# Optimization experiments

Measured on AMD Instinct MI355X. Metric: run time of the kernel, lower is better.

## Reference

```python
import jax, jax.numpy as jnp
import numpy as np

B, T, D = 2, 2048, 1280
H = 20
DH = D // H  # 64
S_PAST = 2048


def setup_inputs() -> dict:
    key = jax.random.key(0)
    ks = jax.random.split(key, 7)
    return {
        "x": jax.random.normal(ks[0], (B, T, D), dtype=jnp.float32),
        "past_K": jax.random.normal(ks[1], (B, H, S_PAST, DH), dtype=jnp.float32),
        "past_V": jax.random.normal(ks[2], (B, H, S_PAST, DH), dtype=jnp.float32),
        "w_q": jax.random.normal(ks[3], (D, D), dtype=jnp.float32),
        "w_k": jax.random.normal(ks[4], (D, D), dtype=jnp.float32),
        "w_v": jax.random.normal(ks[5], (D, D), dtype=jnp.float32),
        "W_o": jax.random.normal(ks[6], (D, D), dtype=jnp.float32),
    }


def reference(x, past_K, past_V, w_q, w_k, w_v, W_o):
    b, t, _ = x.shape
    # projections
    q = x @ w_q  # [B,T,D]
    k = x @ w_k
    v = x @ w_v
    # split heads -> [B,H,T,DH]
    Q = q.reshape(b, t, H, DH).transpose(0, 2, 1, 3)
    K = k.reshape(b, t, H, DH).transpose(0, 2, 1, 3)
    V = v.reshape(b, t, H, DH).transpose(0, 2, 1, 3)
    # concat KV cache along sequence dim
    K = jnp.concatenate([past_K, K], axis=-2)  # [B,H,S_past+T,DH]
    V = jnp.concatenate([past_V, V], axis=-2)
    # attention (no causal mask, matching the original module)
    scores = jnp.einsum("bhtd,bhsd->bhts", Q, K) / jnp.sqrt(jnp.float32(DH))
    attn = jax.nn.softmax(scores, axis=-1)
    values = jnp.einsum("bhts,bhsd->bhtd", attn, V)  # [B,H,T,DH]
    values = values.transpose(0, 2, 1, 3).reshape(b, t, D)
    out = values @ W_o
    return out, K, V
```

## Files before the change

kernel.cpp:

```cpp
#include <hip/hip_runtime.h>

#define NB 2
#define NH 20
#define TT 2048
#define DD 1280
#define DHH 64
#define SP 2048
#define SS 4096
#define MM (NB*TT)

typedef __attribute__((ext_vector_type(8))) short bf16x8;
typedef __attribute__((ext_vector_type(4))) float f32x4;
typedef unsigned short u16;
typedef unsigned int u32;

__device__ __forceinline__ f32x4 mfma16(bf16x8 a, bf16x8 b, f32x4 c) {
  return __builtin_amdgcn_mfma_f32_16x16x32_bf16(a, b, c, 0, 0, 0);
}

__device__ __forceinline__ u16 f2bf(float f) {
  u32 x = __builtin_bit_cast(u32, f);
  x += 0x7fffu + ((x >> 16) & 1u);
  return (u16)(x >> 16);
}
__device__ __forceinline__ float bf2f(u16 u) {
  u32 x = ((u32)u) << 16;
  return __builtin_bit_cast(float, x);
}

__device__ __forceinline__ float fexp2(float x) {
#if __has_builtin(__builtin_amdgcn_exp2f)
  return __builtin_amdgcn_exp2f(x);
#else
  return exp2f(x);
#endif
}

__device__ __forceinline__ u32 cvtpk(float lo, float hi) {
  u32 r;
  asm("v_cvt_pk_bf16_f32 %0, %1, %2" : "=v"(r) : "v"(lo), "v"(hi));
  return r;
}

template<int ROWS>
__device__ __forceinline__ void stage_swz(char* lds, const u16* __restrict__ gsrc,
                                          int ld, int tid) {
  constexpr int ITER = ROWS * 8 / 256;
#pragma unroll
  for (int i = 0; i < ITER; ++i) {
    int id = i * 256 + tid;
    int row = id >> 3, c = id & 7;
    int cs = c ^ (row & 7);
    const u16* src = gsrc + row * ld + cs * 8;
    __builtin_amdgcn_global_load_lds(
        (const __attribute__((address_space(1))) u32*)src,
        (__attribute__((address_space(3))) u32*)(lds + id * 16), 16, 0, 0);
  }
}

__device__ __forceinline__ void gload16(const u16* src, char* ldst) {
  __builtin_amdgcn_global_load_lds(
      (const __attribute__((address_space(1))) u32*)src,
      (__attribute__((address_space(3))) u32*)ldst, 16, 0, 0);
}

__device__ __forceinline__ bf16x8 frag_swz(const char* lds, int row, int cc) {
  return *(const bf16x8*)(lds + row * 128 + ((cc ^ (row & 7)) << 4));
}

__global__ void splitx(const float* __restrict__ x, u16* __restrict__ xh,
                       u16* __restrict__ xl) {
  int i = blockIdx.x * 256 + threadIdx.x;
  float4 v = ((const float4*)x)[i];
  ushort4 hi, lo;
  hi.x = f2bf(v.x); lo.x = f2bf(v.x - bf2f(hi.x));
  hi.y = f2bf(v.y); lo.y = f2bf(v.y - bf2f(hi.y));
  hi.z = f2bf(v.z); lo.z = f2bf(v.z - bf2f(hi.z));
  hi.w = f2bf(v.w); lo.w = f2bf(v.w - bf2f(hi.w));
  ((ushort4*)xh)[i] = hi;
  ((ushort4*)xl)[i] = lo;
}

__global__ void transw(const float* __restrict__ wq, const float* __restrict__ wk,
                       const float* __restrict__ wv, const float* __restrict__ wo,
                       u16* __restrict__ wqkvh, u16* __restrict__ wqkvl,
                       u16* __restrict__ wot) {
  __shared__ float tile[64][65];
  int mat = blockIdx.z;
  const float* src = mat == 0 ? wq : mat == 1 ? wk : mat == 2 ? wv : wo;
  int k0 = blockIdx.x * 64, n0 = blockIdx.y * 64;
  int tid = threadIdx.x;
#pragma unroll
  for (int rep = 0; rep < 16; ++rep) {
    int id = rep * 256 + tid;
    int kl = id >> 6, nl = id & 63;
    tile[nl][kl] = src[(k0 + kl) * DD + n0 + nl];
  }
  __syncthreads();
#pragma unroll
  for (int rep = 0; rep < 16; ++rep) {
    int id = rep * 256 + tid;
    int nl = id >> 6, kl = id & 63;
    float v = tile[nl][kl];
    u16 hi = f2bf(v);
    if (mat < 3) {
      int idx = (mat * DD + n0 + nl) * DD + k0 + kl;
      wqkvh[idx] = hi;
      wqkvl[idx] = f2bf(v - bf2f(hi));
    } else {
      wot[(n0 + nl) * DD + k0 + kl] = hi;
    }
  }
}

__global__ void pastk(const float* __restrict__ pK, float* __restrict__ dK,
                      u16* __restrict__ Kh, u16* __restrict__ Kl) {
  int i = blockIdx.x * 256 + threadIdx.x;
  int e = i * 4;
  int dh = e & 63;
  int s = (e >> 6) & (SP - 1);
  int bh = e >> 17;
  float4 v = *(const float4*)(pK + e);
  int o = (bh * SS + s) * DHH + dh;
  *(float4*)(dK + o) = v;
  ushort4 hi, lo;
  hi.x = f2bf(v.x); lo.x = f2bf(v.x - bf2f(hi.x));
  hi.y = f2bf(v.y); lo.y = f2bf(v.y - bf2f(hi.y));
  hi.z = f2bf(v.z); lo.z = f2bf(v.z - bf2f(hi.z));
  hi.w = f2bf(v.w); lo.w = f2bf(v.w - bf2f(hi.w));
  *(ushort4*)(Kh + o) = hi;
  *(ushort4*)(Kl + o) = lo;
}

__global__ void pastv(const float* __restrict__ pV, float* __restrict__ dV,
                      u16* __restrict__ Vt) {
  __shared__ u16 tile[64][72];
  int bi = blockIdx.x;
  int bh = bi >> 5, st = bi & 31;
  int s0 = st * 64;
  int tid = threadIdx.x;
  const float* src = pV + (bh * SP + s0) * DHH;
  float* dst = dV + (bh * SS + s0) * DHH;
#pragma unroll
  for (int rep = 0; rep < 16; ++rep) {
    int id = rep * 256 + tid;
    int sl = id >> 6, dh = id & 63;
    float v = src[sl * DHH + dh];
    dst[sl * DHH + dh] = v;
    tile[dh][sl] = f2bf(v);
  }
  __syncthreads();
  u16* vdst = Vt + (bh * DHH) * SS + s0;
#pragma unroll
  for (int rep = 0; rep < 4; ++rep) {
    int id = rep * 256 + tid;
    int dh = id >> 4, s4 = (id & 15) * 4;
    ushort4 vv;
    vv.x = tile[dh][s4];     vv.y = tile[dh][s4 + 1];
    vv.z = tile[dh][s4 + 2]; vv.w = tile[dh][s4 + 3];
    *(ushort4*)(vdst + dh * SS + s4) = vv;
  }
}

__launch_bounds__(256, 2)
__global__ void gemm_qkv(const u16* __restrict__ xh, const u16* __restrict__ xl,
                         const u16* __restrict__ wh, const u16* __restrict__ wl,
                         u16* __restrict__ Qh, u16* __restrict__ Ql,
                         u16* __restrict__ Kh, u16* __restrict__ Kl,
                         u16* __restrict__ Vt,
                         float* __restrict__ dK, float* __restrict__ dV) {
  __shared__ __align__(16) char sm[65536];
  char* Ah = sm;          char* Al = sm + 16384;
  char* Bh = sm + 32768;  char* Bl = sm + 49152;
  int tid = threadIdx.x, lane = tid & 63, w = tid >> 6;
  int wm = w >> 1, wn = w & 1;
  int r15 = lane & 15, grp = lane >> 4;
  int mBase = blockIdx.x * 128;
  int by = blockIdx.y;
  int nGlob = by * 128;
  const bool split = (by < 20);
  f32x4 acc[4][4] = {};
  const u16* aH = xh + mBase * DD;
  const u16* aL = xl + mBase * DD;
  const u16* bH = wh + nGlob * DD;
  const u16* bL = wl + nGlob * DD;
  for (int k0 = 0; k0 < DD; k0 += 64) {
    stage_swz<128>(Ah, aH + k0, DD, tid);
    stage_swz<128>(Bh, bH + k0, DD, tid);
    if (split) {
      stage_swz<128>(Al, aL + k0, DD, tid);
      stage_swz<128>(Bl, bL + k0, DD, tid);
    }
    __syncthreads();
#pragma unroll
    for (int kk = 0; kk < 2; ++kk) {
      int cc = kk * 4 + grp;
      bf16x8 fah[4], fal[4], fbh[4], fbl[4];
#pragma unroll
      for (int i = 0; i < 4; ++i) {
        int ra = wm * 64 + i * 16 + r15;
        fah[i] = frag_swz(Ah, ra, cc);
        int rb = wn * 64 + i * 16 + r15;
        fbh[i] = frag_swz(Bh, rb, cc);
        if (split) {
          fal[i] = frag_swz(Al, ra, cc);
          fbl[i] = frag_swz(Bl, rb, cc);
        }
      }
      if (split) {
#pragma unroll
        for (int i = 0; i < 4; ++i)
#pragma unroll
          for (int j = 0; j < 4; ++j) {
            acc[i][j] = mfma16(fah[i], fbh[j], acc[i][j]);
            acc[i][j] = mfma16(fah[i], fbl[j], acc[i][j]);
            acc[i][j] = mfma16(fal[i], fbh[j], acc[i][j]);
          }
      } else {
#pragma unroll
        for (int i = 0; i < 4; ++i)
#pragma unroll
          for (int j = 0; j < 4; ++j)
            acc[i][j] = mfma16(fah[i], fbh[j], acc[i][j]);
      }
    }
    __syncthreads();
  }
  int proj = by / 10;
  int nb = (by % 10) * 128 + wn * 64;
#pragma unroll
  for (int i = 0; i < 4; ++i)
#pragma unroll
    for (int j = 0; j < 4; ++j)
#pragma unroll
      for (int r = 0; r < 4; ++r) {
        int m = mBase + wm * 64 + i * 16 + grp * 4 + r;
        int n = nb + j * 16 + r15;
        float v = acc[i][j][r];
        int b = m >> 11, t = m & 2047;
        int h = n >> 6, dh = n & 63;
        int bhh = b * NH + h;
        if (proj == 0) {
          float q = v * 0.180336880111f;
          u16 hi = f2bf(q);
          int idx = (bhh * TT + t) * DHH + dh;
          Qh[idx] = hi;
          Ql[idx] = f2bf(q - bf2f(hi));
        } else if (proj == 1) {
          int idx = (bhh * SS + SP + t) * DHH + dh;
          dK[idx] = v;
          u16 hi = f2bf(v);
          Kh[idx] = hi;
          Kl[idx] = f2bf(v - bf2f(hi));
        } else {
          int idx = (bhh * SS + SP + t) * DHH + dh;
          dV[idx] = v;
          Vt[(bhh * DHH + dh) * SS + SP + t] = f2bf(v);
        }
      }
}

__launch_bounds__(256, 2)
__global__ void attn(const u16* __restrict__ Qh, const u16* __restrict__ Ql,
                     const u16* __restrict__ Kh, const u16* __restrict__ Kl,
                     const u16* __restrict__ Vt, u16* __restrict__ ao) {
  __shared__ __align__(16) char Ks[8192];
  __shared__ __align__(16) char Kls[8192];
  __shared__ __align__(16) char Vs[8192];
  __shared__ __align__(16) u16 Pw[4][16][72];
  __shared__ __align__(16) float bc[4][16];
  int bi = blockIdx.x;
  int bh = bi >> 4, qt4 = bi & 15;
  int q0 = qt4 * 128;
  int tid = threadIdx.x, lane = tid & 63, w = tid >> 6;
  int r15 = lane & 15, grp = lane >> 4;
  int qbase = q0 + w * 32;
  bf16x8 fqh[2][2], fql[2][2];
#pragma unroll
  for (int qt = 0; qt < 2; ++qt) {
    int qrow = qbase + qt * 16 + r15;
    const u16* qb = Qh + (bh * TT + qrow) * DHH + grp * 8;
    const u16* qbl = Ql + (bh * TT + qrow) * DHH + grp * 8;
    fqh[qt][0] = *(const bf16x8*)qb;   fqh[qt][1] = *(const bf16x8*)(qb + 32);
    fql[qt][0] = *(const bf16x8*)qbl;  fql[qt][1] = *(const bf16x8*)(qbl + 32);
  }
  float mrun[2] = {-1e30f, -1e30f};
  float lrun[2] = {0.f, 0.f};
  f32x4 oacc[2][4] = {};
  int id0 = tid, id1 = 256 + tid;
  int r0 = id0 >> 3, c0 = id0 & 7;
  int r1 = id1 >> 3, c1 = id1 & 7;
  const u16* kh0 = Kh + bh * SS * DHH + r0 * DHH + (c0 ^ (r0 & 7)) * 8;
  const u16* kh1 = Kh + bh * SS * DHH + r1 * DHH + (c1 ^ (r1 & 7)) * 8;
  const u16* kl0 = Kl + bh * SS * DHH + r0 * DHH + (c0 ^ (r0 & 7)) * 8;
  const u16* kl1 = Kl + bh * SS * DHH + r1 * DHH + (c1 ^ (r1 & 7)) * 8;
  const u16* v0 = Vt + bh * DHH * SS + r0 * SS + (c0 ^ (r0 & 7)) * 8;
  const u16* v1 = Vt + bh * DHH * SS + r1 * SS + (c1 ^ (r1 & 7)) * 8;
  char* dK0 = Ks + id0 * 16;  char* dK1 = Ks + id1 * 16;
  char* dL0 = Kls + id0 * 16; char* dL1 = Kls + id1 * 16;
  char* dV0 = Vs + id0 * 16;  char* dV1 = Vs + id1 * 16;

  for (int it = 0; it < SS / 64; ++it) {
    gload16(kh0, dK0); gload16(kh1, dK1);
    gload16(kl0, dL0); gload16(kl1, dL1);
    gload16(v0, dV0);  gload16(v1, dV1);
    kh0 += 64 * DHH; kh1 += 64 * DHH;
    kl0 += 64 * DHH; kl1 += 64 * DHH;
    v0 += 64; v1 += 64;
    __syncthreads();
#pragma unroll
    for (int qt = 0; qt < 2; ++qt) {
      f32x4 st[4];
      __builtin_amdgcn_s_setprio(1);
#pragma unroll
      for (int kt = 0; kt < 4; ++kt) {
        f32x4 a = {0.f, 0.f, 0.f, 0.f};
#pragma unroll
        for (int ks = 0; ks < 2; ++ks) {
          int cc = ks * 4 + grp;
          bf16x8 kfh = frag_swz(Ks, kt * 16 + r15, cc);
          bf16x8 kfl = frag_swz(Kls, kt * 16 + r15, cc);
          a = mfma16(kfh, fqh[qt][ks], a);
          a = mfma16(kfh, fql[qt][ks], a);
          a = mfma16(kfl, fqh[qt][ks], a);
        }
        st[kt] = a;
      }
      __builtin_amdgcn_s_setprio(0);
      float cm = fmaxf(fmaxf(fmaxf(st[0][0], st[0][1]), fmaxf(st[0][2], st[0][3])),
                       fmaxf(fmaxf(st[1][0], st[1][1]), fmaxf(st[1][2], st[1][3])));
      cm = fmaxf(cm, fmaxf(fmaxf(fmaxf(st[2][0], st[2][1]), fmaxf(st[2][2], st[2][3])),
                           fmaxf(fmaxf(st[3][0], st[3][1]), fmaxf(st[3][2], st[3][3]))));
      cm = fmaxf(cm, __shfl_xor(cm, 16));
      cm = fmaxf(cm, __shfl_xor(cm, 32));
      if (!__all(cm <= mrun[qt] + 8.f)) {
        float mnew = fmaxf(mrun[qt], cm);
        float sc = fexp2(mrun[qt] - mnew);
        lrun[qt] *= sc;
        mrun[qt] = mnew;
        if (grp == 0) bc[w][r15] = sc;
        f32x4 scv = *(const f32x4*)&bc[w][grp * 4];
#pragma unroll
        for (int d = 0; d < 4; ++d) {
          oacc[qt][d][0] *= scv[0]; oacc[qt][d][1] *= scv[1];
          oacc[qt][d][2] *= scv[2]; oacc[qt][d][3] *= scv[3];
        }
      }
      float m = mrun[qt];
      float ps = 0.f;
#pragma unroll
      for (int kt = 0; kt < 4; ++kt)
#pragma unroll
        for (int r = 0; r < 4; ++r) {
          float p = fexp2(st[kt][r] - m);
          st[kt][r] = p;
          ps += p;
        }
      ps += __shfl_xor(ps, 16);
      ps += __shfl_xor(ps, 32);
      lrun[qt] += ps;
#pragma unroll
      for (int kt = 0; kt < 4; ++kt) {
        u32 w0 = cvtpk(st[kt][0], st[kt][1]);
        u32 w1 = cvtpk(st[kt][2], st[kt][3]);
        uint2 pk = {w0, w1};
        *(uint2*)&Pw[w][r15][kt * 16 + grp * 4] = pk;
      }
      bf16x8 pa0 = *(const bf16x8*)&Pw[w][r15][grp * 8];
      bf16x8 pa1 = *(const bf16x8*)&Pw[w][r15][32 + grp * 8];
      __builtin_amdgcn_s_setprio(1);
#pragma unroll
      for (int d = 0; d < 4; ++d) {
        bf16x8 vf0 = frag_swz(Vs, d * 16 + r15, grp);
        bf16x8 vf1 = frag_swz(Vs, d * 16 + r15, 4 + grp);
        oacc[qt][d] = mfma16(pa0, vf0, oacc[qt][d]);
        oacc[qt][d] = mfma16(pa1, vf1, oacc[qt][d]);
      }
      __builtin_amdgcn_s_setprio(0);
    }
    __syncthreads();
  }
  int b = bh / NH, h = bh % NH;
#pragma unroll
  for (int qt = 0; qt < 2; ++qt) {
    float inv = 1.0f / lrun[qt];
    if (grp == 0) bc[w][r15] = inv;
    f32x4 li = *(const f32x4*)&bc[w][grp * 4];
#pragma unroll
    for (int d = 0; d < 4; ++d)
#pragma unroll
      for (int r = 0; r < 4; ++r) {
        int q = qbase + qt * 16 + grp * 4 + r;
        int col = h * DHH + d * 16 + r15;
        ao[(b * TT + q) * DD + col] = f2bf(oacc[qt][d][r] * li[r]);
      }
  }
}

__launch_bounds__(256, 2)
__global__ void gemm_out(const u16* __restrict__ ao, const u16* __restrict__ wot,
                         float* __restrict__ out) {
  __shared__ __align__(16) char sm[32768];
  char* As = sm;
  char* Bs = sm + 16384;
  int tid = threadIdx.x, lane = tid & 63, w = tid >> 6;
  int wm = w >> 1, wn = w & 1;
  int r15 = lane & 15, grp = lane >> 4;
  int mBase = blockIdx.x * 128, nBase = blockIdx.y * 128;
  f32x4 acc[4][4] = {};
  for (int k0 = 0; k0 < DD; k0 += 64) {
    stage_swz<128>(As, ao + mBase * DD + k0, DD, tid);
    stage_swz<128>(Bs, wot + nBase * DD + k0, DD, tid);
    __syncthreads();
#pragma unroll
    for (int kk = 0; kk < 2; ++kk) {
      int cc = kk * 4 + grp;
      bf16x8 fa[4], fb[4];
#pragma unroll
      for (int i = 0; i < 4; ++i) {
        fa[i] = frag_swz(As, wm * 64 + i * 16 + r15, cc);
        fb[i] = frag_swz(Bs, wn * 64 + i * 16 + r15, cc);
      }
#pragma unroll
      for (int i = 0; i < 4; ++i)
#pragma unroll
        for (int j = 0; j < 4; ++j)
          acc[i][j] = mfma16(fa[i], fb[j], acc[i][j]);
    }
    __syncthreads();
  }
#pragma unroll
  for (int i = 0; i < 4; ++i)
#pragma unroll
    for (int j = 0; j < 4; ++j)
#pragma unroll
      for (int r = 0; r < 4; ++r) {
        int m = mBase + wm * 64 + i * 16 + grp * 4 + r;
        int n = nBase + wn * 64 + j * 16 + r15;
        out[m * DD + n] = acc[i][j][r];
      }
}

extern "C" void kernel_launch(void* const* d_in, const int* in_sizes, int n_in,
                              void* d_out, int out_size, void* d_ws, size_t ws_size,
                              hipStream_t stream) {
  const float* x  = (const float*)d_in[0];
  const float* pK = (const float*)d_in[1];
  const float* pV = (const float*)d_in[2];
  const float* wq = (const float*)d_in[3];
  const float* wk = (const float*)d_in[4];
  const float* wv = (const float*)d_in[5];
  const float* wo = (const float*)d_in[6];

  float* out = (float*)d_out;
  float* dK  = out + NB * TT * DD;
  float* dV  = dK + NB * NH * SS * DHH;

  u16* xh    = (u16*)d_ws;
  u16* xl    = xh + MM * DD;
  u16* wqkvh = xl + MM * DD;
  u16* wqkvl = wqkvh + 3 * DD * DD;
  u16* wot   = wqkvl + 3 * DD * DD;
  u16* Qh    = wot + DD * DD;
  u16* Ql    = Qh + MM * DD;
  u16* Kh    = Ql + MM * DD;
  u16* Kl    = Kh + NB * NH * SS * DHH;
  u16* Vt    = Kl + NB * NH * SS * DHH;
  u16* ao    = xh;

  splitx<<<dim3(MM * DD / 4 / 256), 256, 0, stream>>>(x, xh, xl);
  transw<<<dim3(20, 20, 4), 256, 0, stream>>>(wq, wk, wv, wo, wqkvh, wqkvl, wot);
  pastk<<<dim3(NB * NH * SP * DHH / 4 / 256), 256, 0, stream>>>(pK, dK, Kh, Kl);
  pastv<<<dim3(NB * NH * (SP / 64)), 256, 0, stream>>>(pV, dV, Vt);
  gemm_qkv<<<dim3(32, 30), 256, 0, stream>>>(xh, xl, wqkvh, wqkvl,
                                             Qh, Ql, Kh, Kl, Vt, dK, dV);
  attn<<<dim3(NB * NH * (TT / 128)), 256, 0, stream>>>(Qh, Ql, Kh, Kl, Vt, ao);
  gemm_out<<<dim3(32, 10), 256, 0, stream>>>(ao, wot, out);
}
```

Baseline: 402.0 us.

## Double-buffer LDS staging in QKV GEMM and attention, remap attention blocks to XCDs

The QKV GEMM and the attention kernel now use two LDS buffers. The next tile's global-to-LDS loads are issued before computing on the current tile, and a single vmcnt wait plus barrier ends each step, replacing the two __syncthreads per iteration. The GEMM k-tile shrinks from 64 to 32 with a 4-way swizzle so the doubled buffers fit in the same 64KB. Attention hoists its K fragments out of the q-tile loop and remaps block indices so each XCD works on a contiguous set of heads for L2 locality. The cost is more LDS (attention rises to 48KB plus extras), which may reduce occupancy, and twice as many k-steps in the GEMM.

```diff
diff --git a/kernel.cpp b/kernel.cpp
--- a/kernel.cpp
+++ b/kernel.cpp
@@ -42,6 +42,9 @@
   return r;
 }
 
+#define VMCNT0() asm volatile("s_waitcnt vmcnt(0)" ::: "memory")
+#define BAR() __builtin_amdgcn_s_barrier()
+
 template<int ROWS>
 __device__ __forceinline__ void stage_swz(char* lds, const u16* __restrict__ gsrc,
                                           int ld, int tid) {
@@ -66,6 +69,9 @@
 
 __device__ __forceinline__ bf16x8 frag_swz(const char* lds, int row, int cc) {
   return *(const bf16x8*)(lds + row * 128 + ((cc ^ (row & 7)) << 4));
+}
+__device__ __forceinline__ bf16x8 frag32(const char* lds, int row, int cc) {
+  return *(const bf16x8*)(lds + row * 64 + ((cc ^ (row & 3)) << 4));
 }
 
 __global__ void splitx(const float* __restrict__ x, u16* __restrict__ xh,
@@ -170,8 +176,6 @@
                          u16* __restrict__ Vt,
                          float* __restrict__ dK, float* __restrict__ dV) {
   __shared__ __align__(16) char sm[65536];
-  char* Ah = sm;          char* Al = sm + 16384;
-  char* Bh = sm + 32768;  char* Bl = sm + 49152;
   int tid = threadIdx.x, lane = tid & 63, w = tid >> 6;
   int wm = w >> 1, wn = w & 1;
   int r15 = lane & 15, grp = lane >> 4;
@@ -180,52 +184,72 @@
   int nGlob = by * 128;
   const bool split = (by < 20);
   f32x4 acc[4][4] = {};
+  int id0 = tid, id1 = 256 + tid;
+  int r0 = id0 >> 2, c0 = id0 & 3;
+  int r1 = id1 >> 2, c1 = id1 & 3;
+  int so0 = r0 * DD + (c0 ^ (r0 & 3)) * 8;
+  int so1 = r1 * DD + (c1 ^ (r1 & 3)) * 8;
   const u16* aH = xh + mBase * DD;
   const u16* aL = xl + mBase * DD;
   const u16* bH = wh + nGlob * DD;
   const u16* bL = wl + nGlob * DD;
-  for (int k0 = 0; k0 < DD; k0 += 64) {
-    stage_swz<128>(Ah, aH + k0, DD, tid);
-    stage_swz<128>(Bh, bH + k0, DD, tid);
+  int do0 = id0 * 16, do1 = id1 * 16;
+
+  auto stage = [&](int buf, int k0) {
+    char* b = sm + buf * 32768;
+    gload16(aH + k0 + so0, b + do0);
+    gload16(aH + k0 + so1, b + do1);
+    gload16(bH + k0 + so0, b + 16384 + do0);
+    gload16(bH + k0 + so1, b + 16384 + do1);
     if (split) {
-      stage_swz<128>(Al, aL + k0, DD, tid);
-      stage_swz<128>(Bl, bL + k0, DD, tid);
+      gload16(aL + k0 + so0, b + 8192 + do0);
+      gload16(aL + k0 + so1, b + 8192 + do1);
+      gload16(bL + k0 + so0, b + 24576 + do0);
+      gload16(bL + k0 + so1, b + 24576 + do1);
     }
-    __syncthreads();
-#pragma unroll
-    for (int kk = 0; kk < 2; ++kk) {
-      int cc = kk * 4 + grp;
-      bf16x8 fah[4], fal[4], fbh[4], fbl[4];
-#pragma unroll
-      for (int i = 0; i < 4; ++i) {
-        int ra = wm * 64 + i * 16 + r15;
-        fah[i] = frag_swz(Ah, ra, cc);
-        int rb = wn * 64 + i * 16 + r15;
-        fbh[i] = frag_swz(Bh, rb, cc);
-        if (split) {
-          fal[i] = frag_swz(Al, ra, cc);
-          fbl[i] = frag_swz(Bl, rb, cc);
+  };
+  auto compute = [&](int buf) {
+    const char* b = sm + buf * 32768;
+    bf16x8 fah[4], fal[4], fbh[4], fbl[4];
+#pragma unroll
+    for (int i = 0; i < 4; ++i) {
+      fah[i] = frag32(b, wm * 64 + i * 16 + r15, grp);
+      fbh[i] = frag32(b + 16384, wn * 64 + i * 16 + r15, grp);
+      if (split) {
+        fal[i] = frag32(b + 8192, wm * 64 + i * 16 + r15, grp);
+        fbl[i] = frag32(b + 24576, wn * 64 + i * 16 + r15, grp);
+      }
+    }
+    __builtin_amdgcn_s_setprio(1);
+    if (split) {
+#pragma unroll
+      for (int i = 0; i < 4; ++i)
+#pragma unroll
+        for (int j = 0; j < 4; ++j) {
+          acc[i][j] = mfma16(fah[i], fbh[j], acc[i][j]);
+          acc[i][j] = mfma16(fah[i], fbl[j], acc[i][j]);
+          acc[i][j] = mfma16(fal[i], fbh[j], acc[i][j]);
         }
-      }
-      if (split) {
-#pragma unroll
-        for (int i = 0; i < 4; ++i)
-#pragma unroll
-          for (int j = 0; j < 4; ++j) {
-            acc[i][j] = mfma16(fah[i], fbh[j], acc[i][j]);
-            acc[i][j] = mfma16(fah[i], fbl[j], acc[i][j]);
-            acc[i][j] = mfma16(fal[i], fbh[j], acc[i][j]);
-          }
-      } else {
-#pragma unroll
-        for (int i = 0; i < 4; ++i)
-#pragma unroll
-          for (int j = 0; j < 4; ++j)
-            acc[i][j] = mfma16(fah[i], fbh[j], acc[i][j]);
-      }
+    } else {
+#pragma unroll
+      for (int i = 0; i < 4; ++i)
+#pragma unroll
+        for (int j = 0; j < 4; ++j)
+          acc[i][j] = mfma16(fah[i], fbh[j], acc[i][j]);
     }
-    __syncthreads();
-  }
+    __builtin_amdgcn_s_setprio(0);
+  };
+
+  stage(0, 0);
+  VMCNT0(); BAR();
+#pragma unroll 2
+  for (int step = 0; step < 39; ++step) {
+    stage((step + 1) & 1, (step + 1) * 32);
+    compute(step & 1);
+    VMCNT0(); BAR();
+  }
+  compute(1);
+
   int proj = by / 10;
   int nb = (by % 10) * 128 + wn * 64;
 #pragma unroll
@@ -264,14 +288,13 @@
 __global__ void attn(const u16* __restrict__ Qh, const u16* __restrict__ Ql,
                      const u16* __restrict__ Kh, const u16* __restrict__ Kl,
                      const u16* __restrict__ Vt, u16* __restrict__ ao) {
-  __shared__ __align__(16) char Ks[8192];
-  __shared__ __align__(16) char Kls[8192];
-  __shared__ __align__(16) char Vs[8192];
+  __shared__ __align__(16) char smem[49152];
   __shared__ __align__(16) u16 Pw[4][16][72];
   __shared__ __align__(16) float bc[4][16];
-  int bi = blockIdx.x;
-  int bh = bi >> 4, qt4 = bi & 15;
-  int q0 = qt4 * 128;
+  int d = blockIdx.x;
+  int xcd = d & 7, sl = d >> 3;
+  int bh = xcd * 5 + (sl >> 4);
+  int q0 = (sl & 15) * 128;
   int tid = threadIdx.x, lane = tid & 63, w = tid >> 6;
   int r15 = lane & 15, grp = lane >> 4;
   int qbase = q0 + w * 32;
@@ -296,18 +319,29 @@
   const u16* kl1 = Kl + bh * SS * DHH + r1 * DHH + (c1 ^ (r1 & 7)) * 8;
   const u16* v0 = Vt + bh * DHH * SS + r0 * SS + (c0 ^ (r0 & 7)) * 8;
   const u16* v1 = Vt + bh * DHH * SS + r1 * SS + (c1 ^ (r1 & 7)) * 8;
-  char* dK0 = Ks + id0 * 16;  char* dK1 = Ks + id1 * 16;
-  char* dL0 = Kls + id0 * 16; char* dL1 = Kls + id1 * 16;
-  char* dV0 = Vs + id0 * 16;  char* dV1 = Vs + id1 * 16;
-
-  for (int it = 0; it < SS / 64; ++it) {
-    gload16(kh0, dK0); gload16(kh1, dK1);
-    gload16(kl0, dL0); gload16(kl1, dL1);
-    gload16(v0, dV0);  gload16(v1, dV1);
+  int do0 = id0 * 16, do1 = id1 * 16;
+
+  auto stage = [&](int buf) {
+    char* b = smem + buf * 24576;
+    gload16(kh0, b + do0);          gload16(kh1, b + do1);
+    gload16(kl0, b + 8192 + do0);   gload16(kl1, b + 8192 + do1);
+    gload16(v0, b + 16384 + do0);   gload16(v1, b + 16384 + do1);
     kh0 += 64 * DHH; kh1 += 64 * DHH;
     kl0 += 64 * DHH; kl1 += 64 * DHH;
     v0 += 64; v1 += 64;
-    __syncthreads();
+  };
+  auto compute = [&](int buf) {
+    const char* cb = smem + buf * 24576;
+    const char* Klc = cb + 8192;
+    const char* Vsc = cb + 16384;
+    bf16x8 kf[4][2], klf[4][2];
+#pragma unroll
+    for (int kt = 0; kt < 4; ++kt)
+#pragma unroll
+      for (int ks = 0; ks < 2; ++ks) {
+        kf[kt][ks] = frag_swz(cb, kt * 16 + r15, ks * 4 + grp);
+        klf[kt][ks] = frag_swz(Klc, kt * 16 + r15, ks * 4 + grp);
+      }
 #pragma unroll
     for (int qt = 0; qt < 2; ++qt) {
       f32x4 st[4];
@@ -317,12 +351,9 @@
         f32x4 a = {0.f, 0.f, 0.f, 0.f};
 #pragma unroll
         for (int ks = 0; ks < 2; ++ks) {
-          int cc = ks * 4 + grp;
-          bf16x8 kfh = frag_swz(Ks, kt * 16 + r15, cc);
-          bf16x8 kfl = frag_swz(Kls, kt * 16 + r15, cc);
-          a = mfma16(kfh, fqh[qt][ks], a);
-          a = mfma16(kfh, fql[qt][ks], a);
-          a = mfma16(kfl, fqh[qt][ks], a);
+          a = mfma16(kf[kt][ks], fqh[qt][ks], a);
+          a = mfma16(kf[kt][ks], fql[qt][ks], a);
+          a = mfma16(klf[kt][ks], fqh[qt][ks], a);
         }
         st[kt] = a;
       }
@@ -341,9 +372,9 @@
         if (grp == 0) bc[w][r15] = sc;
         f32x4 scv = *(const f32x4*)&bc[w][grp * 4];
 #pragma unroll
-        for (int d = 0; d < 4; ++d) {
-          oacc[qt][d][0] *= scv[0]; oacc[qt][d][1] *= scv[1];
-          oacc[qt][d][2] *= scv[2]; oacc[qt][d][3] *= scv[3];
+        for (int dd = 0; dd < 4; ++dd) {
+          oacc[qt][dd][0] *= scv[0]; oacc[qt][dd][1] *= scv[1];
+          oacc[qt][dd][2] *= scv[2]; oacc[qt][dd][3] *= scv[3];
         }
       }
       float m = mrun[qt];
@@ -370,16 +401,26 @@
       bf16x8 pa1 = *(const bf16x8*)&Pw[w][r15][32 + grp * 8];
       __builtin_amdgcn_s_setprio(1);
 #pragma unroll
-      for (int d = 0; d < 4; ++d) {
-        bf16x8 vf0 = frag_swz(Vs, d * 16 + r15, grp);
-        bf16x8 vf1 = frag_swz(Vs, d * 16 + r15, 4 + grp);
-        oacc[qt][d] = mfma16(pa0, vf0, oacc[qt][d]);
-        oacc[qt][d] = mfma16(pa1, vf1, oacc[qt][d]);
+      for (int dd = 0; dd < 4; ++dd) {
+        bf16x8 vf0 = frag_swz(Vsc, dd * 16 + r15, grp);
+        bf16x8 vf1 = frag_swz(Vsc, dd * 16 + r15, 4 + grp);
+        oacc[qt][dd] = mfma16(pa0, vf0, oacc[qt][dd]);
+        oacc[qt][dd] = mfma16(pa1, vf1, oacc[qt][dd]);
       }
       __builtin_amdgcn_s_setprio(0);
     }
-    __syncthreads();
-  }
+  };
+
+  stage(0);
+  VMCNT0(); BAR();
+#pragma unroll 2
+  for (int it = 0; it < SS / 64 - 1; ++it) {
+    stage((it + 1) & 1);
+    compute(it & 1);
+    VMCNT0(); BAR();
+  }
+  compute(1);
+
   int b = bh / NH, h = bh % NH;
 #pragma unroll
   for (int qt = 0; qt < 2; ++qt) {
@@ -387,12 +428,12 @@
     if (grp == 0) bc[w][r15] = inv;
     f32x4 li = *(const f32x4*)&bc[w][grp * 4];
 #pragma unroll
-    for (int d = 0; d < 4; ++d)
+    for (int dd = 0; dd < 4; ++dd)
 #pragma unroll
       for (int r = 0; r < 4; ++r) {
         int q = qbase + qt * 16 + grp * 4 + r;
-        int col = h * DHH + d * 16 + r15;
-        ao[(b * TT + q) * DD + col] = f2bf(oacc[qt][d][r] * li[r]);
+        int col = h * DHH + dd * 16 + r15;
+        ao[(b * TT + q) * DD + col] = f2bf(oacc[qt][dd][r] * li[r]);
       }
   }
 }
```

Measured after the change: 437.3 us. +8.8%, slower.
